# Optimization experiments

Measured on AMD Instinct MI355X. Metric: run time of the kernel, lower is better.

The kernel has to match this reference:

```python
import jax, jax.numpy as jnp
import numpy as np

EMBED_DIM = 1024
NUM_HEADS = 16
HEAD_DIM = EMBED_DIM // NUM_HEADS
ROPE_BASE = 10000.0


def _rope_angles(seq_len, head_dim):
    inv_freq = 1.0 / (ROPE_BASE ** (jnp.arange(0, head_dim, 2, dtype=jnp.float32) / head_dim))  # [D/2]
    pos = jnp.arange(seq_len, dtype=jnp.float32)
    ang = pos[:, None] * inv_freq[None, :]  # [S, D/2]
    return jnp.cos(ang), jnp.sin(ang)


def _apply_rope(t, cos, sin):
    # t: [B, H, S, D]; rotate-half convention
    d2 = t.shape[-1] // 2
    t1, t2 = t[..., :d2], t[..., d2:]
    return jnp.concatenate([t1 * cos - t2 * sin, t2 * cos + t1 * sin], axis=-1)


def setup_inputs() -> dict:
    key = jax.random.key(0)
    ks = jax.random.split(key, 6)
    B, S, E = 1, 4096, EMBED_DIM
    x = jax.random.normal(ks[0], (B, S, E), dtype=jnp.float32)
    # causal mask: True means masked-out (upper triangle above diagonal)
    mask = jnp.triu(jnp.ones((S, S), dtype=bool), k=1)[None, None, :, :]
    scale = 0.02
    wqkv_w = jax.random.normal(ks[1], (E, 3 * E), dtype=jnp.float32) * scale
    wqkv_b = jax.random.normal(ks[2], (3 * E,), dtype=jnp.float32) * scale
    out_w = jax.random.normal(ks[3], (E, E), dtype=jnp.float32) * scale
    out_b = jax.random.normal(ks[4], (E,), dtype=jnp.float32) * scale
    return {"x": x, "mask": mask, "wqkv_w": wqkv_w, "wqkv_b": wqkv_b, "out_w": out_w, "out_b": out_b}


def reference(x, mask, wqkv_w, wqkv_b, out_w, out_b):
    B, S, E = x.shape
    H, D = NUM_HEADS, HEAD_DIM
    qkv = x @ wqkv_w + wqkv_b  # [B, S, 3E]
    q, k, v = jnp.split(qkv, 3, axis=-1)
    # [B, S, E] -> [B, H, S, D]
    q = q.reshape(B, S, H, D).transpose(0, 2, 1, 3)
    k = k.reshape(B, S, H, D).transpose(0, 2, 1, 3)
    v = v.reshape(B, S, H, D).transpose(0, 2, 1, 3)
    cos, sin = _rope_angles(S, D)  # [S, D/2]
    q = _apply_rope(q, cos, sin)
    k = _apply_rope(k, cos, sin)
    scores = jnp.einsum('bhqd,bhkd->bhqk', q, k) * (D ** -0.5)  # [B, H, S, S]
    scores = jnp.where(mask[:, :, -S:, :], -jnp.inf, scores)
    weights = jax.nn.softmax(scores, axis=-1)
    ctx = jnp.einsum('bhqk,bhkd->bhqd', weights, v)  # [B, H, S, D]
    ctx = ctx.transpose(0, 2, 1, 3).reshape(B, S, E)
    return ctx @ out_w + out_b
```

## Files before the change

kernel.cpp:

```cpp
#include <hip/hip_runtime.h>
#include <hip/hip_bf16.h>
#include <math.h>

#define S_LEN 4096
#define EMB   1024
#define E3    3072
#define NH    16
#define HD    64

typedef unsigned short u16;
typedef short          bfrag __attribute__((ext_vector_type(8)));
typedef float          ffrag __attribute__((ext_vector_type(4)));
typedef unsigned short us8   __attribute__((ext_vector_type(8)));
typedef unsigned short us4   __attribute__((ext_vector_type(4)));

__device__ __forceinline__ u16 f2bf(float f) {
    union { float f; unsigned u; } v; v.f = f;
    unsigned r = v.u + 0x7fffu + ((v.u >> 16) & 1u);
    return (u16)(r >> 16);
}
__device__ __forceinline__ float bf2f(u16 b) {
    union { unsigned u; float f; } v; v.u = ((unsigned)b) << 16;
    return v.f;
}
__device__ __forceinline__ unsigned pack_bf16_trunc(float lo, float hi) {
    union { float f; unsigned u; } a, b; a.f = lo; b.f = hi;
    return __builtin_amdgcn_perm(b.u, a.u, 0x07060302u);
}
__device__ __forceinline__ void gld16(const void* g, void* l) {
    __builtin_amdgcn_global_load_lds(
        (const __attribute__((address_space(1))) unsigned int*)g,
        (__attribute__((address_space(3))) unsigned int*)l, 16, 0, 0);
}

__global__ __launch_bounds__(256)
void cast_bf16_kernel(const float* __restrict__ in, u16* __restrict__ out) {
    const size_t i = ((size_t)blockIdx.x * 256 + threadIdx.x) * 8;
    float4 a = *(const float4*)(in + i);
    float4 b = *(const float4*)(in + i + 4);
    us8 o;
    o[0]=f2bf(a.x); o[1]=f2bf(a.y); o[2]=f2bf(a.z); o[3]=f2bf(a.w);
    o[4]=f2bf(b.x); o[5]=f2bf(b.y); o[6]=f2bf(b.z); o[7]=f2bf(b.w);
    *(us8*)(out + i) = o;
}

__global__ __launch_bounds__(256)
void transpose_cast_kernel(const float* __restrict__ in, u16* __restrict__ out,
                           int R, int C) {
    __shared__ u16 T[64][72];
    const int r0 = blockIdx.x * 64, c0 = blockIdx.y * 64;
    const int t = threadIdx.x;
    const int rr = t >> 2, cc = (t & 3) * 16;

    const float* ip = in + (size_t)(r0 + rr) * C + c0 + cc;
    u16 tmp[16];
    #pragma unroll
    for (int i4 = 0; i4 < 4; i4++) {
        float4 v = ((const float4*)ip)[i4];
        tmp[4*i4+0]=f2bf(v.x); tmp[4*i4+1]=f2bf(v.y);
        tmp[4*i4+2]=f2bf(v.z); tmp[4*i4+3]=f2bf(v.w);
    }
    #pragma unroll
    for (int i8 = 0; i8 < 2; i8++) {
        us8 vv;
        #pragma unroll
        for (int j = 0; j < 8; j++) vv[j] = tmp[8*i8+j];
        *(us8*)&T[rr][cc + 8*i8] = vv;
    }
    __syncthreads();

    const int oc = t >> 2, orr = (t & 3) * 16;
    u16 ot[16];
    #pragma unroll
    for (int j = 0; j < 16; j++) ot[j] = T[orr + j][oc];
    u16* op = out + (size_t)(c0 + oc) * R + r0 + orr;
    #pragma unroll
    for (int i8 = 0; i8 < 2; i8++) {
        us8 vv;
        #pragma unroll
        for (int j = 0; j < 8; j++) vv[j] = ot[8*i8+j];
        *(us8*)(op + 8*i8) = vv;
    }
}

template <int OUT_BF16, int NT, int ROPE, int MINW>
__global__ __launch_bounds__(256, MINW)
void gemm_bt_kernel(const u16* __restrict__ A, const u16* __restrict__ Bt,
                    const float* __restrict__ bias, void* __restrict__ Cv,
                    u16* __restrict__ vtp, int M, int N, int K) {
    constexpr int BN = 32 * NT;
    constexpr int WS = 16 * NT;
    __shared__ u16 As[2][128][32];
    __shared__ u16 Bs[2][BN][32];

    const int tid = threadIdx.x;
    const int w = tid >> 6, L = tid & 63;
    const int col = L & 15, quad = L >> 4;
    const int wm = w & 1, wn = w >> 1;
    const int m0 = blockIdx.x * 128, n0 = blockIdx.y * BN;

    ffrag acc[4][NT];
    #pragma unroll
    for (int a = 0; a < 4; a++)
        #pragma unroll
        for (int b = 0; b < NT; b++)
            #pragma unroll
            for (int r = 0; r < 4; r++) acc[a][b][r] = 0.f;

    const int srow = L >> 2;
    const int schk = L & 3;

    #pragma unroll
    for (int t = 0; t < 2; t++) {
        const int rg = (2 * w + t) * 16;
        gld16(A + (size_t)(m0 + rg + srow) * K + schk * 8, &As[0][rg][0]);
    }
    #pragma unroll
    for (int t = 0; t < NT / 2; t++) {
        const int rg = (w * (NT / 2) + t) * 16;
        gld16(Bt + (size_t)(n0 + rg + srow) * K + schk * 8, &Bs[0][rg][0]);
    }
    __syncthreads();

    int buf = 0;
    for (int k0 = 0; k0 < K; k0 += 32, buf ^= 1) {
        if (k0 + 32 < K) {
            #pragma unroll
            for (int t = 0; t < 2; t++) {
                const int rg = (2 * w + t) * 16;
                gld16(A + (size_t)(m0 + rg + srow) * K + k0 + 32 + schk * 8,
                      &As[buf ^ 1][rg][0]);
            }
            #pragma unroll
            for (int t = 0; t < NT / 2; t++) {
                const int rg = (w * (NT / 2) + t) * 16;
                gld16(Bt + (size_t)(n0 + rg + srow) * K + k0 + 32 + schk * 8,
                      &Bs[buf ^ 1][rg][0]);
            }
        }

        bfrag af[4], bf[NT];
        #pragma unroll
        for (int mt = 0; mt < 4; mt++)
            af[mt] = *(const bfrag*)&As[buf][64 * wm + 16 * mt + col][8 * quad];
        #pragma unroll
        for (int nt = 0; nt < NT; nt++)
            bf[nt] = *(const bfrag*)&Bs[buf][WS * wn + 16 * nt + col][8 * quad];
        #pragma unroll
        for (int mt = 0; mt < 4; mt++)
            #pragma unroll
            for (int nt = 0; nt < NT; nt++)
                acc[mt][nt] = __builtin_amdgcn_mfma_f32_16x16x32_bf16(
                    af[mt], bf[nt], acc[mt][nt], 0, 0, 0);

        __syncthreads();
    }

    float bv[NT];
    #pragma unroll
    for (int nt = 0; nt < NT; nt++) bv[nt] = bias[n0 + WS * wn + 16 * nt + col];

    if (ROPE && n0 < 2 * EMB) {
        const float SCq = (n0 < EMB) ? 0.125f * 1.44269504088896f : 1.0f;
        const float C = 13.287712379549449f / 32.0f;
        float invf[2];
        invf[0] = exp2f(-(float)col * C);
        invf[1] = exp2f(-(float)(col + 16) * C);
        #pragma unroll
        for (int mt = 0; mt < 4; mt++) {
            #pragma unroll
            for (int r = 0; r < 4; r++) {
                const int mrow = m0 + 64 * wm + 16 * mt + 4 * quad + r;
                const float fs = (float)mrow;
                u16* cp = (u16*)Cv + (size_t)mrow * N + n0 + 64 * wn + col;
                #pragma unroll
                for (int pr = 0; pr < 2; pr++) {
                    float sn, cs;
                    sincosf(fs * invf[pr], &sn, &cs);
                    const float t1 = acc[mt][pr][r] + bv[pr];
                    const float t2 = acc[mt][pr + 2][r] + bv[pr + 2];
                    cp[16 * pr]      = f2bf((t1 * cs - t2 * sn) * SCq);
                    cp[16 * pr + 32] = f2bf((t2 * cs + t1 * sn) * SCq);
                }
            }
        }
    } else if (ROPE) {
        #pragma unroll
        for (int nt = 0; nt < NT; nt++) {
            const int dg = n0 - 2 * EMB + WS * wn + 16 * nt + col;
            #pragma unroll
            for (int mt = 0; mt < 4; mt++) {
                const int s0 = m0 + 64 * wm + 16 * mt + 4 * quad;
                us4 pk;
                #pragma unroll
                for (int r = 0; r < 4; r++) pk[r] = f2bf(acc[mt][nt][r] + bv[nt]);
                *(us4*)&vtp[(size_t)dg * S_LEN + s0] = pk;
            }
        }
    } else {
        #pragma unroll
        for (int mt = 0; mt < 4; mt++) {
            #pragma unroll
            for (int r = 0; r < 4; r++) {
                const int m = m0 + 64 * wm + 16 * mt + 4 * quad + r;
                #pragma unroll
                for (int nt = 0; nt < NT; nt++) {
                    const int n = n0 + WS * wn + 16 * nt + col;
                    const float val = acc[mt][nt][r] + bv[nt];
                    if (OUT_BF16) ((u16*)Cv)[(size_t)m * N + n] = f2bf(val);
                    else          ((float*)Cv)[(size_t)m * N + n] = val;
                }
            }
        }
    }
}

__global__ __launch_bounds__(256, 3)
void flash9_kernel(const u16* __restrict__ qkvb, const u16* __restrict__ vt,
                   u16* __restrict__ ctxb, u16* __restrict__ pO,
                   float* __restrict__ pL) {
    __shared__ u16 QP[4][32][64];
    __shared__ u16 Ks[2][64][64];
    __shared__ u16 Vs[2][64][64];

    const int id = blockIdx.x;
    const int x  = id & 7;
    const int r  = id >> 3;
    const int h  = x + 8 * (r >= 48);
    const int rr = (r >= 48) ? (r - 48) : r;

    int type, qi, kt0, cnt;
    if (rr < 16)      { type = 1; qi = 31 - rr;        kt0 = 0;      cnt = qi + 1; }
    else if (rr < 32) { type = 2; qi = 31 - (rr - 16); kt0 = qi + 1; cnt = qi + 1; }
    else              { type = 0; qi = 15 - (rr - 32); kt0 = 0;      cnt = 2 * qi + 2; }
    const int q0 = qi * 128;

    const int tid = threadIdx.x;
    const int w = tid >> 6, L = tid & 63;
    const int col = L & 15, quad = L >> 4;
    const int lr = L >> 3, lp = L & 7;
    const int lc = lp ^ lr;

    const bool domask = (type != 1);
    const int nwt = cnt - ((domask && w < 2) ? 1 : 0);

    const size_t kArow = (size_t)(16 * w + lr) * E3 + EMB + h * HD + lc * 8;
    const size_t vArow = ((size_t)h * HD + 16 * w + lr) * S_LEN + lc * 8;
    const size_t kt0off  = (size_t)kt0 * 64 * E3;
    const size_t vt0off  = (size_t)kt0 * 64;

    #pragma unroll
    for (int u = 0; u < 4; u++)
        gld16(qkvb + (size_t)(q0 + 32 * w + 8 * u + lr) * E3 + h * HD + lc * 8,
              &QP[w][8 * u][0]);
    #pragma unroll
    for (int u = 0; u < 2; u++) {
        gld16(qkvb + kArow + kt0off + (size_t)(8 * u) * E3,
              &Ks[0][16 * w + 8 * u][0]);
        gld16(vt + vArow + vt0off + (size_t)(8 * u) * S_LEN,
              &Vs[0][16 * w + 8 * u][0]);
    }
    __syncthreads();

    bfrag qf[2][2];
    #pragma unroll
    for (int i = 0; i < 2; i++)
        #pragma unroll
        for (int ks = 0; ks < 2; ks++)
            qf[i][ks] = *(const bfrag*)
                ((const char*)&QP[w][16 * i + col][0] +
                 16 * ((4 * ks + quad) ^ (col & 7)));

    bfrag ones;
    #pragma unroll
    for (int i = 0; i < 8; i++) ones[i] = (short)0x3F80;

    ffrag o[4][2], ol[2];
    #pragma unroll
    for (int d4 = 0; d4 < 4; d4++)
        #pragma unroll
        for (int i = 0; i < 2; i++)
            #pragma unroll
            for (int r2 = 0; r2 < 4; r2++) o[d4][i][r2] = 0.f;
    #pragma unroll
    for (int i = 0; i < 2; i++)
        #pragma unroll
        for (int r2 = 0; r2 < 4; r2++) ol[i][r2] = 0.f;

    #pragma unroll 1
    for (int t = 0; t < cnt; t++) {
        const int buf = t & 1;
        if (t + 1 < cnt) {
            const size_t ko = kArow + kt0off + (size_t)(t + 1) * 64 * E3;
            const size_t vo = vArow + vt0off + (size_t)(t + 1) * 64;
            #pragma unroll
            for (int u = 0; u < 2; u++) {
                gld16(qkvb + ko + (size_t)(8 * u) * E3,
                      &Ks[buf ^ 1][16 * w + 8 * u][0]);
                gld16(vt + vo + (size_t)(8 * u) * S_LEN,
                      &Vs[buf ^ 1][16 * w + 8 * u][0]);
            }
        }

        if (t < nwt) {
            ffrag st[4][2];
            #pragma unroll
            for (int t4 = 0; t4 < 4; t4++)
                #pragma unroll
                for (int i = 0; i < 2; i++)
                    #pragma unroll
                    for (int r2 = 0; r2 < 4; r2++) st[t4][i][r2] = 0.f;
            #pragma unroll
            for (int ks = 0; ks < 2; ks++) {
                bfrag kf[4];
                #pragma unroll
                for (int t4 = 0; t4 < 4; t4++)
                    kf[t4] = *(const bfrag*)
                        &Ks[buf][16 * t4 + col][(((4 * ks + quad) ^ (col & 7)) * 8)];
                #pragma unroll
                for (int t4 = 0; t4 < 4; t4++)
                    #pragma unroll
                    for (int i = 0; i < 2; i++)
                        st[t4][i] = __builtin_amdgcn_mfma_f32_16x16x32_bf16(
                            kf[t4], qf[i][ks], st[t4][i], 0, 0, 0);
            }

            if (domask && t == nwt - 1) {
                #pragma unroll
                for (int i = 0; i < 2; i++) {
                    const int qrel = 32 * (w & 1) + 16 * i + col;
                    #pragma unroll
                    for (int t4 = 0; t4 < 4; t4++) {
                        const int key0 = 16 * t4 + 4 * quad;
                        #pragma unroll
                        for (int r2 = 0; r2 < 4; r2++)
                            if (key0 + r2 > qrel) st[t4][i][r2] = -3.0e38f;
                    }
                }
            }

            #pragma unroll
            for (int i = 0; i < 2; i++) {
                const int prow = 16 * i + col;
                #pragma unroll
                for (int t4 = 0; t4 < 4; t4++) {
                    float pr[4];
                    #pragma unroll
                    for (int r2 = 0; r2 < 4; r2++) pr[r2] = exp2f(st[t4][i][r2]);
                    uint2 pk;
                    pk.x = pack_bf16_trunc(pr[0], pr[1]);
                    pk.y = pack_bf16_trunc(pr[2], pr[3]);
                    const int c2 = (2 * t4 + (quad >> 1)) ^ (col & 7);
                    *(uint2*)((char*)&QP[w][prow][0] + 16 * c2 + 8 * (quad & 1)) = pk;
                }
            }

            #pragma unroll
            for (int ks = 0; ks < 2; ks++) {
                bfrag vf[4];
                #pragma unroll
                for (int d4 = 0; d4 < 4; d4++)
                    vf[d4] = *(const bfrag*)
                        &Vs[buf][16 * d4 + col][(((4 * ks + quad) ^ (col & 7)) * 8)];
                bfrag pf[2];
                #pragma unroll
                for (int i = 0; i < 2; i++)
                    pf[i] = *(const bfrag*)
                        ((const char*)&QP[w][16 * i + col][0] +
                         16 * ((4 * ks + quad) ^ (col & 7)));
                #pragma unroll
                for (int d4 = 0; d4 < 4; d4++)
                    #pragma unroll
                    for (int i = 0; i < 2; i++)
                        o[d4][i] = __builtin_amdgcn_mfma_f32_16x16x32_bf16(
                            vf[d4], pf[i], o[d4][i], 0, 0, 0);
                #pragma unroll
                for (int i = 0; i < 2; i++)
                    ol[i] = __builtin_amdgcn_mfma_f32_16x16x32_bf16(
                        ones, pf[i], ol[i], 0, 0, 0);
            }
        }

        __syncthreads();
    }

    if (type == 0) {
        #pragma unroll
        for (int i = 0; i < 2; i++) {
            const float inv = 1.0f / ol[i][0];
            const int qg = q0 + 32 * w + 16 * i + col;
            #pragma unroll
            for (int d4 = 0; d4 < 4; d4++) {
                us4 pk;
                #pragma unroll
                for (int r2 = 0; r2 < 4; r2++) pk[r2] = f2bf(o[d4][i][r2] * inv);
                *(us4*)&ctxb[(size_t)qg * EMB + h * HD + 16 * d4 + 4 * quad] = pk;
            }
        }
    } else {
        const int half = type - 1;
        const int g = h * 16 + (qi - 16);
        u16* po = pO + (size_t)half * 256 * 128 * 64 + (size_t)g * 128 * 64;
        float* pl = pL + half * 256 * 128 + g * 128;
        #pragma unroll
        for (int i = 0; i < 2; i++) {
            const int qrow = 32 * w + 16 * i + col;
            #pragma unroll
            for (int d4 = 0; d4 < 4; d4++) {
                us4 pk;
                #pragma unroll
                for (int r2 = 0; r2 < 4; r2++) pk[r2] = f2bf(o[d4][i][r2]);
                *(us4*)&po[(size_t)qrow * 64 + 16 * d4 + 4 * quad] = pk;
            }
            if (quad == 0) pl[qrow] = ol[i][0];
        }
    }
}

__global__ __launch_bounds__(256)
void combine_kernel(const u16* __restrict__ pO, const float* __restrict__ pL,
                    u16* __restrict__ ctxb) {
    const int g = blockIdx.x;
    const int h = g >> 4, qi = 16 + (g & 15);
    const int t = threadIdx.x;
    const int q = t >> 1, dh = (t & 1) * 32;

    const float la = pL[g * 128 + q];
    const float lb = pL[256 * 128 + g * 128 + q];
    const float inv = 1.0f / (la + lb);

    const u16* a = pO + ((size_t)g * 128 + q) * 64 + dh;
    const u16* b = a + (size_t)256 * 128 * 64;
    u16* op = ctxb + (size_t)(qi * 128 + q) * EMB + h * HD + dh;

    #pragma unroll
    for (int j = 0; j < 4; j++) {
        us8 va = *(const us8*)(a + 8 * j);
        us8 vb = *(const us8*)(b + 8 * j);
        us8 vo;
        #pragma unroll
        for (int e = 0; e < 8; e++)
            vo[e] = f2bf((bf2f(va[e]) + bf2f(vb[e])) * inv);
        *(us8*)(op + 8 * j) = vo;
    }
}

extern "C" void kernel_launch(void* const* d_in, const int* in_sizes, int n_in,
                              void* d_out, int out_size, void* d_ws, size_t ws_size,
                              hipStream_t stream) {
    const float* x      = (const float*)d_in[0];
    const float* wqkv_w = (const float*)d_in[2];
    const float* wqkv_b = (const float*)d_in[3];
    const float* out_w  = (const float*)d_in[4];
    const float* out_b  = (const float*)d_in[5];
    float* out = (float*)d_out;

    u16* qkvb = (u16*)d_ws;
    u16* ctxb = qkvb + (size_t)S_LEN * E3;
    u16* xb   = ctxb + (size_t)S_LEN * EMB;
    u16* wt   = xb   + (size_t)S_LEN * EMB;
    u16* owt  = wt   + (size_t)E3 * EMB;
    u16* vtb  = owt  + (size_t)EMB * EMB;

    u16*   pO = xb;
    float* pL = (float*)wt;

    dim3 blk(256);

    cast_bf16_kernel<<<dim3(S_LEN * EMB / (256 * 8)), blk, 0, stream>>>(x, xb);
    transpose_cast_kernel<<<dim3(EMB / 64, E3 / 64), blk, 0, stream>>>(
        wqkv_w, wt, EMB, E3);
    transpose_cast_kernel<<<dim3(EMB / 64, EMB / 64), blk, 0, stream>>>(
        out_w, owt, EMB, EMB);

    gemm_bt_kernel<1, 4, 1, 3><<<dim3(S_LEN / 128, E3 / 128), blk, 0, stream>>>(
        xb, wt, wqkv_b, qkvb, vtb, S_LEN, E3, EMB);

    flash9_kernel<<<dim3(768), blk, 0, stream>>>(qkvb, vtb, ctxb, pO, pL);
    combine_kernel<<<dim3(256), blk, 0, stream>>>(pO, pL, ctxb);

    gemm_bt_kernel<0, 2, 0, 2><<<dim3(S_LEN / 128, EMB / 64), blk, 0, stream>>>(
        ctxb, owt, out_b, out, nullptr, S_LEN, EMB, EMB);
}
```

Baseline: 257.1 us.

## Rebalance causal flash attention by splitting long query tiles into three KV chunks

The flash kernel's work decomposition changes. Query tiles 22-31 now split their KV range into 3 chunks, tiles 11-21 into 2 chunks, and short tiles stay whole, launched as 1008 blocks instead of 768. Partial outputs and row sums go to per-head slots that a generalized combine kernel sums and normalizes. The goal is shorter, more even block lengths so the tail of the causal workload is better balanced across CUs. The cost is more partial-output traffic, a larger combine pass, and scratch space that now extends into the weight-transpose buffer.

Measured after the change: 249.4 us. 1.03x faster.

```diff
diff --git a/kernel.cpp b/kernel.cpp
--- a/kernel.cpp
+++ b/kernel.cpp
@@ -7,6 +7,9 @@
 #define E3    3072
 #define NH    16
 #define HD    64
+
+#define SLOTS_PER_HEAD 52
+#define NSLOTS         832
 
 typedef unsigned short u16;
 typedef short          bfrag __attribute__((ext_vector_type(8)));
@@ -216,23 +219,30 @@
 }
 
 __global__ __launch_bounds__(256, 3)
-void flash9_kernel(const u16* __restrict__ qkvb, const u16* __restrict__ vt,
-                   u16* __restrict__ ctxb, u16* __restrict__ pO,
-                   float* __restrict__ pL) {
+void flash10_kernel(const u16* __restrict__ qkvb, const u16* __restrict__ vt,
+                    u16* __restrict__ ctxb, u16* __restrict__ pO,
+                    float* __restrict__ pL) {
     __shared__ u16 QP[4][32][64];
     __shared__ u16 Ks[2][64][64];
     __shared__ u16 Vs[2][64][64];
 
     const int id = blockIdx.x;
     const int x  = id & 7;
-    const int r  = id >> 3;
-    const int h  = x + 8 * (r >= 48);
-    const int rr = (r >= 48) ? (r - 48) : r;
-
-    int type, qi, kt0, cnt;
-    if (rr < 16)      { type = 1; qi = 31 - rr;        kt0 = 0;      cnt = qi + 1; }
-    else if (rr < 32) { type = 2; qi = 31 - (rr - 16); kt0 = qi + 1; cnt = qi + 1; }
-    else              { type = 0; qi = 15 - (rr - 32); kt0 = 0;      cnt = 2 * qi + 2; }
+    const int tt = id >> 3;
+    const int h  = x + 8 * (tt & 1);
+    const int o  = tt >> 1;
+
+    int qi, ch, nc;
+    if (o < 30)      { qi = 31 - o / 3;        ch = o % 3;        nc = 3; }
+    else if (o < 33) { qi = 10 - (o - 30);     ch = 0;            nc = 1; }
+    else if (o < 55) { const int oo = o - 33;  qi = 21 - oo / 2;  ch = oo & 1; nc = 2; }
+    else             { qi = 7 - (o - 55);      ch = 0;            nc = 1; }
+
+    const int total = 2 * qi + 2;
+    const int Lc    = (total + nc - 1) / nc;
+    const int kt0   = ch * Lc;
+    const int cnt   = min(Lc, total - kt0);
+    const bool lastch = (kt0 + cnt == total);
     const int q0 = qi * 128;
 
     const int tid = threadIdx.x;
@@ -241,7 +251,7 @@
     const int lr = L >> 3, lp = L & 7;
     const int lc = lp ^ lr;
 
-    const bool domask = (type != 1);
+    const bool domask = lastch;
     const int nwt = cnt - ((domask && w < 2) ? 1 : 0);
 
     const size_t kArow = (size_t)(16 * w + lr) * E3 + EMB + h * HD + lc * 8;
@@ -275,13 +285,13 @@
     #pragma unroll
     for (int i = 0; i < 8; i++) ones[i] = (short)0x3F80;
 
-    ffrag o[4][2], ol[2];
+    ffrag o_[4][2], ol[2];
     #pragma unroll
     for (int d4 = 0; d4 < 4; d4++)
         #pragma unroll
         for (int i = 0; i < 2; i++)
             #pragma unroll
-            for (int r2 = 0; r2 < 4; r2++) o[d4][i][r2] = 0.f;
+            for (int r2 = 0; r2 < 4; r2++) o_[d4][i][r2] = 0.f;
     #pragma unroll
     for (int i = 0; i < 2; i++)
         #pragma unroll
@@ -372,8 +382,8 @@
                 for (int d4 = 0; d4 < 4; d4++)
                     #pragma unroll
                     for (int i = 0; i < 2; i++)
-                        o[d4][i] = __builtin_amdgcn_mfma_f32_16x16x32_bf16(
-                            vf[d4], pf[i], o[d4][i], 0, 0, 0);
+                        o_[d4][i] = __builtin_amdgcn_mfma_f32_16x16x32_bf16(
+                            vf[d4], pf[i], o_[d4][i], 0, 0, 0);
                 #pragma unroll
                 for (int i = 0; i < 2; i++)
                     ol[i] = __builtin_amdgcn_mfma_f32_16x16x32_bf16(
@@ -384,7 +394,7 @@
         __syncthreads();
     }
 
-    if (type == 0) {
+    if (nc == 1) {
         #pragma unroll
         for (int i = 0; i < 2; i++) {
             const float inv = 1.0f / ol[i][0];
@@ -393,15 +403,15 @@
             for (int d4 = 0; d4 < 4; d4++) {
                 us4 pk;
                 #pragma unroll
-                for (int r2 = 0; r2 < 4; r2++) pk[r2] = f2bf(o[d4][i][r2] * inv);
+                for (int r2 = 0; r2 < 4; r2++) pk[r2] = f2bf(o_[d4][i][r2] * inv);
                 *(us4*)&ctxb[(size_t)qg * EMB + h * HD + 16 * d4 + 4 * quad] = pk;
             }
         }
     } else {
-        const int half = type - 1;
-        const int g = h * 16 + (qi - 16);
-        u16* po = pO + (size_t)half * 256 * 128 * 64 + (size_t)g * 128 * 64;
-        float* pl = pL + half * 256 * 128 + g * 128;
+        const int jj = (qi <= 21) ? (qi - 11) * 2 + ch : 22 + (qi - 22) * 3 + ch;
+        const int slot = h * SLOTS_PER_HEAD + jj;
+        u16* po = pO + (size_t)slot * (128 * 64);
+        float* pl = pL + slot * 128;
         #pragma unroll
         for (int i = 0; i < 2; i++) {
             const int qrow = 32 * w + 16 * i + col;
@@ -409,7 +419,7 @@
             for (int d4 = 0; d4 < 4; d4++) {
                 us4 pk;
                 #pragma unroll
-                for (int r2 = 0; r2 < 4; r2++) pk[r2] = f2bf(o[d4][i][r2]);
+                for (int r2 = 0; r2 < 4; r2++) pk[r2] = f2bf(o_[d4][i][r2]);
                 *(us4*)&po[(size_t)qrow * 64 + 16 * d4 + 4 * quad] = pk;
             }
             if (quad == 0) pl[qrow] = ol[i][0];
@@ -421,26 +431,33 @@
 void combine_kernel(const u16* __restrict__ pO, const float* __restrict__ pL,
                     u16* __restrict__ ctxb) {
     const int g = blockIdx.x;
-    const int h = g >> 4, qi = 16 + (g & 15);
+    const int h = g / 21, qq = g % 21;
+    const int qi = 11 + qq;
+    const int nc = (qi <= 21) ? 2 : 3;
+    const int jj0 = (qi <= 21) ? (qi - 11) * 2 : 22 + (qi - 22) * 3;
+    const int slot0 = h * SLOTS_PER_HEAD + jj0;
+
     const int t = threadIdx.x;
     const int q = t >> 1, dh = (t & 1) * 32;
 
-    const float la = pL[g * 128 + q];
-    const float lb = pL[256 * 128 + g * 128 + q];
-    const float inv = 1.0f / (la + lb);
-
-    const u16* a = pO + ((size_t)g * 128 + q) * 64 + dh;
-    const u16* b = a + (size_t)256 * 128 * 64;
+    float l = 0.f;
+    for (int p = 0; p < nc; p++) l += pL[(slot0 + p) * 128 + q];
+    const float inv = 1.0f / l;
+
     u16* op = ctxb + (size_t)(qi * 128 + q) * EMB + h * HD + dh;
 
     #pragma unroll
     for (int j = 0; j < 4; j++) {
-        us8 va = *(const us8*)(a + 8 * j);
-        us8 vb = *(const us8*)(b + 8 * j);
+        float s[8] = {0.f, 0.f, 0.f, 0.f, 0.f, 0.f, 0.f, 0.f};
+        for (int p = 0; p < nc; p++) {
+            const us8 va = *(const us8*)
+                (pO + ((size_t)(slot0 + p) * 128 + q) * 64 + dh + 8 * j);
+            #pragma unroll
+            for (int e = 0; e < 8; e++) s[e] += bf2f(va[e]);
+        }
         us8 vo;
         #pragma unroll
-        for (int e = 0; e < 8; e++)
-            vo[e] = f2bf((bf2f(va[e]) + bf2f(vb[e])) * inv);
+        for (int e = 0; e < 8; e++) vo[e] = f2bf(s[e] * inv);
         *(us8*)(op + 8 * j) = vo;
     }
 }
@@ -463,7 +480,7 @@
     u16* vtb  = owt  + (size_t)EMB * EMB;
 
     u16*   pO = xb;
-    float* pL = (float*)wt;
+    float* pL = (float*)(xb + (size_t)NSLOTS * 128 * 64);
 
     dim3 blk(256);
 
@@ -476,8 +493,8 @@
     gemm_bt_kernel<1, 4, 1, 3><<<dim3(S_LEN / 128, E3 / 128), blk, 0, stream>>>(
         xb, wt, wqkv_b, qkvb, vtb, S_LEN, E3, EMB);
 
-    flash9_kernel<<<dim3(768), blk, 0, stream>>>(qkvb, vtb, ctxb, pO, pL);
-    combine_kernel<<<dim3(256), blk, 0, stream>>>(pO, pL, ctxb);
+    flash10_kernel<<<dim3(1008), blk, 0, stream>>>(qkvb, vtb, ctxb, pO, pL);
+    combine_kernel<<<dim3(336), blk, 0, stream>>>(pO, pL, ctxb);
 
     gemm_bt_kernel<0, 2, 0, 2><<<dim3(S_LEN / 128, EMB / 64), blk, 0, stream>>>(
         ctxb, owt, out_b, out, nullptr, S_LEN, EMB, EMB);
```
